# Performance work log

Measured on AMD Instinct MI355X. Metric: run time of the kernel, lower is better.

Reference implementation:

```python
import jax, jax.numpy as jnp
import numpy as np

S = 8192
Q_PARAM = 256
V_PARAM = 256
SCALE = 1.0 / np.sqrt(float(Q_PARAM)).astype(np.float32)


def setup_inputs() -> dict:
    key = jax.random.key(0)
    ks = jax.random.split(key, 12)
    init = lambda k, shape, fan_in: jax.random.uniform(k, shape, jnp.float32, -1.0, 1.0) / np.sqrt(float(fan_in))
    return {
        "query": jax.random.normal(ks[0], (S, Q_PARAM), jnp.float32),
        "key": jax.random.normal(ks[1], (S, Q_PARAM), jnp.float32),
        "value": jax.random.normal(ks[2], (S, V_PARAM), jnp.float32),
        "mask": jax.random.uniform(ks[3], (S, S), jnp.float32),
        "Wq": init(ks[4], (Q_PARAM, Q_PARAM), Q_PARAM),
        "bq": init(ks[5], (Q_PARAM,), Q_PARAM),
        "Wk": init(ks[6], (Q_PARAM, Q_PARAM), Q_PARAM),
        "bk": init(ks[7], (Q_PARAM,), Q_PARAM),
        "Wv": init(ks[8], (V_PARAM, V_PARAM), V_PARAM),
        "bv": init(ks[9], (V_PARAM,), V_PARAM),
        "Wo": init(ks[10], (V_PARAM, V_PARAM), V_PARAM),
        "bo": init(ks[11], (V_PARAM,), V_PARAM),
    }


def reference(query, key, value, mask, Wq, bq, Wk, bk, Wv, bv, Wo, bo):
    # torch nn.Linear: y = x @ W.T + b
    q = query @ Wq.T + bq          # [S, q]
    k = key @ Wk.T + bk            # [S, q]
    v = value @ Wv.T + bv          # [S, v]
    scores = q @ k.T               # [S, S]
    masked = scores * mask         # multiplicative mask BEFORE softmax
    h = jax.nn.softmax(masked * SCALE, axis=1)
    h = h @ v                      # [S, v]
    return h @ Wo.T + bo
```

## Files before the change

### kernel.cpp

```cpp
#include <hip/hip_runtime.h>


#define S 8192
#define NSPLIT 4
#define BM 64
#define BN 32
#define KSPLIT_LEN (S / NSPLIT)
#define NTILES (KSPLIT_LEN / BN)

typedef unsigned short ushort_t;
typedef __attribute__((ext_vector_type(8))) __bf16 bf16x8;
typedef __attribute__((ext_vector_type(4))) float f32x4;
typedef __attribute__((ext_vector_type(4))) ushort_t ushort4_t;
typedef __attribute__((ext_vector_type(8))) ushort_t ushort8_t;

typedef const __attribute__((address_space(1))) unsigned int* gas_u32;
typedef __attribute__((address_space(3))) unsigned int* las_u32;

__device__ __forceinline__ ushort_t f2bf(float f) {
  unsigned u = __builtin_bit_cast(unsigned, f);
  u += 0x7FFFu + ((u >> 16) & 1u);
  return (ushort_t)(u >> 16);
}

__device__ __forceinline__ bf16x8 pack8(f32x4 a, f32x4 b) {
  ushort8_t u;
  u[0] = f2bf(a[0]); u[1] = f2bf(a[1]); u[2] = f2bf(a[2]); u[3] = f2bf(a[3]);
  u[4] = f2bf(b[0]); u[5] = f2bf(b[1]); u[6] = f2bf(b[2]); u[7] = f2bf(b[3]);
  return __builtin_bit_cast(bf16x8, u);
}

__global__ __launch_bounds__(256) void wconv_kernel(
    const float* __restrict__ w0, const float* __restrict__ w1,
    const float* __restrict__ w2, const float* __restrict__ w3,
    ushort_t* __restrict__ o0, ushort_t* __restrict__ o1,
    ushort_t* __restrict__ o2, ushort_t* __restrict__ o3) {
  const int m = blockIdx.y;
  const float* w = (m == 0) ? w0 : (m == 1) ? w1 : (m == 2) ? w2 : w3;
  ushort_t* o = (m == 0) ? o0 : (m == 1) ? o1 : (m == 2) ? o2 : o3;
  const int idx = (blockIdx.x * 256 + threadIdx.x) * 4;
  f32x4 v = *(const f32x4*)(w + idx);
  ushort4_t p;
  p[0] = f2bf(v[0]); p[1] = f2bf(v[1]); p[2] = f2bf(v[2]); p[3] = f2bf(v[3]);
  *(ushort4_t*)(o + idx) = p;
}

template <int IN_BF16, int OUT_MODE>
__global__ __launch_bounds__(256) void proj_kernel(const void* __restrict__ inp,
                                                   const ushort_t* __restrict__ Wb,
                                                   const float* __restrict__ bias,
                                                   void* __restrict__ outp) {
  const int tid = threadIdx.x;
  const int lane = tid & 63;
  const int w = tid >> 6;
  const int lr = lane & 15, lg = lane >> 4;
  const int brow0 = blockIdx.x * 64;
  const int row0 = brow0 + w * 16;
  const int col0 = blockIdx.y * 64;

  f32x4 acc[4] = {};
  const int arow = row0 + lr;
  const int kb = lg * 8;

  bf16x8 af[8];
#pragma unroll
  for (int ks = 0; ks < 8; ++ks) {
    if (IN_BF16) {
      af[ks] = *(const bf16x8*)((const ushort_t*)inp + (size_t)arow * 256 + ks * 32 + kb);
    } else {
      const float* ap = (const float*)inp + (size_t)arow * 256 + ks * 32 + kb;
      af[ks] = pack8(*(const f32x4*)ap, *(const f32x4*)(ap + 4));
    }
  }

#pragma unroll
  for (int ks = 0; ks < 8; ++ks) {
#pragma unroll
    for (int n = 0; n < 4; ++n) {
      bf16x8 bb = *(const bf16x8*)(Wb + (size_t)(col0 + 16 * n + lr) * 256 + ks * 32 + kb);
      acc[n] = __builtin_amdgcn_mfma_f32_16x16x32_bf16(af[ks], bb, acc[n], 0, 0, 0);
    }
  }

  if constexpr (OUT_MODE == 1) {
    __shared__ __align__(16) ushort_t tb[64 * 68];
#pragma unroll
    for (int n = 0; n < 4; ++n) {
      const int col = col0 + 16 * n + lr;
      const float bv = bias[col];
      const int cl = 16 * n + lr;
      const int rowl = w * 16 + lg * 4;
      ushort4_t pk;
#pragma unroll
      for (int r = 0; r < 4; ++r) pk[r] = f2bf(acc[n][r] + bv);
      *(ushort4_t*)&tb[cl * 68 + rowl] = pk;
    }
    __syncthreads();
    ushort_t* o = (ushort_t*)outp;
#pragma unroll
    for (int i = 0; i < 4; ++i) {
      int chunk = i * 256 + tid;
      int c = chunk >> 4;
      int off = (chunk & 15) * 4;
      ushort4_t v0 = *(const ushort4_t*)&tb[c * 68 + off];
      *(ushort4_t*)(o + (size_t)(col0 + c) * S + brow0 + off) = v0;
    }
  } else {
#pragma unroll
    for (int n = 0; n < 4; ++n) {
      const int col = col0 + 16 * n + lr;
      const float bv = bias[col];
      const int rbase = row0 + lg * 4;
      if (OUT_MODE == 0) {
        ushort_t* o = (ushort_t*)outp;
#pragma unroll
        for (int r = 0; r < 4; ++r)
          o[(size_t)(rbase + r) * 256 + col] = f2bf(acc[n][r] + bv);
      } else {
        float* o = (float*)outp;
#pragma unroll
        for (int r = 0; r < 4; ++r)
          o[(size_t)(rbase + r) * 256 + col] = acc[n][r] + bv;
      }
    }
  }
}

__global__ __launch_bounds__(256) void flash_kernel(
    const ushort_t* __restrict__ qb, const ushort_t* __restrict__ kbm,
    const ushort_t* __restrict__ vtb, const float* __restrict__ mask,
    float* __restrict__ Opart, float* __restrict__ lpart) {
  __shared__ __align__(16) ushort_t kt[2 * BN * 256];
  __shared__ __align__(16) ushort_t vt[2 * 256 * BN];
  __shared__ __align__(16) ushort_t pb[4][16 * BN];

  const int tid = threadIdx.x;
  const int lane = tid & 63;
  const int w = tid >> 6;
  const int lr = lane & 15, lg = lane >> 4;
  const int split = blockIdx.y;
  const int kvbase = split * KSPLIT_LEN;
  const int qrow0 = blockIdx.x * BM + w * 16;

  bf16x8 qf[8];
#pragma unroll
  for (int ks = 0; ks < 8; ++ks)
    qf[ks] = *(const bf16x8*)(qb + (size_t)(qrow0 + lr) * 256 + ks * 32 + lg * 8);

  const float* mrow[4];
#pragma unroll
  for (int r = 0; r < 4; ++r)
    mrow[r] = mask + (size_t)(qrow0 + lg * 4 + r) * S + lr;

  f32x4 oacc[16] = {};
  float lsum[4] = {0.f, 0.f, 0.f, 0.f};

  const int pa_off = lr * (BN * 2) + lg * 16;
  const int vt_swz = ((lg ^ (lane & 3)) << 4);
  ushort_t* pbw = &pb[w][0];

  auto stage = [&](int b, int kv0) {
#pragma unroll
    for (int it = 0; it < 4; ++it) {
      int chunk = it * 256 + (w << 6) + lane;
      int r = chunk >> 5;
      int c = (chunk & 31) ^ (r & 7);
      const ushort_t* src = kbm + (size_t)(kv0 + r) * 256 + c * 8;
      __builtin_amdgcn_global_load_lds((gas_u32)src,
                                       (las_u32)(kt + b * 8192 + it * 2048 + w * 512), 16, 0, 0);
    }
#pragma unroll
    for (int it = 0; it < 4; ++it) {
      int chunk = it * 256 + (w << 6) + lane;
      int r = chunk >> 2;
      int c = (chunk & 3) ^ (r & 3);
      const ushort_t* src = vtb + (size_t)r * S + kv0 + c * 8;
      __builtin_amdgcn_global_load_lds((gas_u32)src,
                                       (las_u32)(vt + b * 8192 + it * 2048 + w * 512), 16, 0, 0);
    }
  };

  stage(0, kvbase);
  float mcur[8];
#pragma unroll
  for (int n = 0; n < 2; ++n)
#pragma unroll
    for (int r = 0; r < 4; ++r)
      mcur[n * 4 + r] = __builtin_nontemporal_load(mrow[r] + kvbase + 16 * n);
  __syncthreads();

  for (int t = 0; t < NTILES; ++t) {
    const int cur = t & 1;
    const int tn = (t + 1 < NTILES) ? (t + 1) : t;
    const int kvn = kvbase + tn * BN;

    stage(cur ^ 1, kvn);
    float mnext[8];
#pragma unroll
    for (int n = 0; n < 2; ++n)
#pragma unroll
      for (int r = 0; r < 4; ++r)
        mnext[n * 4 + r] = __builtin_nontemporal_load(mrow[r] + kvn + 16 * n);

    const char* ktc = (const char*)kt + cur * 16384;
    f32x4 sacc[2] = {};
#pragma unroll
    for (int ks = 0; ks < 8; ++ks) {
#pragma unroll
      for (int n = 0; n < 2; ++n) {
        int addr = ((16 * n + lr) << 9) + ((((ks << 2) + lg) ^ (lane & 7)) << 4);
        bf16x8 bk = *(const bf16x8*)(ktc + addr);
        sacc[n] = __builtin_amdgcn_mfma_f32_16x16x32_bf16(qf[ks], bk, sacc[n], 0, 0, 0);
      }
    }

#pragma unroll
    for (int n = 0; n < 2; ++n) {
#pragma unroll
      for (int r = 0; r < 4; ++r) {
        float p = __builtin_amdgcn_exp2f(sacc[n][r] * (mcur[n * 4 + r] * 0.09016844005556021f));
        lsum[r] += p;
        pbw[(lg * 4 + r) * BN + 16 * n + lr] = f2bf(p);
      }
    }

    const char* vtc = (const char*)vt + cur * 16384;
    bf16x8 pa = *(const bf16x8*)((const char*)pbw + pa_off);
#pragma unroll
    for (int nd = 0; nd < 16; ++nd) {
      bf16x8 bv = *(const bf16x8*)(vtc + nd * 1024 + lr * 64 + vt_swz);
      oacc[nd] = __builtin_amdgcn_mfma_f32_16x16x32_bf16(pa, bv, oacc[nd], 0, 0, 0);
    }

#pragma unroll
    for (int i = 0; i < 8; ++i) mcur[i] = mnext[i];
    __syncthreads();
  }

#pragma unroll
  for (int r = 0; r < 4; ++r) {
    float v = lsum[r];
    v += __shfl_xor(v, 1);
    v += __shfl_xor(v, 2);
    v += __shfl_xor(v, 4);
    v += __shfl_xor(v, 8);
    lsum[r] = v;
  }
  const int absrow0 = qrow0 + lg * 4;
  if (lr == 0) {
#pragma unroll
    for (int r = 0; r < 4; ++r)
      lpart[(size_t)split * S + absrow0 + r] = lsum[r];
  }
#pragma unroll
  for (int r = 0; r < 4; ++r) {
    float* orow = Opart + ((size_t)split * S + absrow0 + r) * 256 + lr;
#pragma unroll
    for (int nd = 0; nd < 16; ++nd) orow[nd * 16] = oacc[nd][r];
  }
}

__global__ __launch_bounds__(256) void combine_kernel(const float* __restrict__ Opart,
                                                      const float* __restrict__ lpart,
                                                      ushort_t* __restrict__ hb) {
  const int row = blockIdx.x;
  const int d = threadIdx.x;
  float L = 0.f, acc = 0.f;
#pragma unroll
  for (int s2 = 0; s2 < NSPLIT; ++s2) {
    L += lpart[(size_t)s2 * S + row];
    acc += Opart[((size_t)s2 * S + row) * 256 + d];
  }
  hb[(size_t)row * 256 + d] = f2bf(acc / L);
}

extern "C" void kernel_launch(void* const* d_in, const int* in_sizes, int n_in,
                              void* d_out, int out_size, void* d_ws, size_t ws_size,
                              hipStream_t stream) {
  const float* query = (const float*)d_in[0];
  const float* key   = (const float*)d_in[1];
  const float* value = (const float*)d_in[2];
  const float* mask  = (const float*)d_in[3];
  const float* Wq = (const float*)d_in[4];
  const float* bq = (const float*)d_in[5];
  const float* Wk = (const float*)d_in[6];
  const float* bk = (const float*)d_in[7];
  const float* Wv = (const float*)d_in[8];
  const float* bv = (const float*)d_in[9];
  const float* Wo = (const float*)d_in[10];
  const float* bo = (const float*)d_in[11];

  char* ws = (char*)d_ws;
  ushort_t* qb  = (ushort_t*)(ws);
  ushort_t* kb  = (ushort_t*)(ws + ((size_t)4  << 20));
  ushort_t* vtb = (ushort_t*)(ws + ((size_t)8  << 20));
  ushort_t* hb  = (ushort_t*)(ws + ((size_t)12 << 20));
  float* Opart  = (float*)(ws + ((size_t)16 << 20));
  float* lpart  = (float*)(ws + ((size_t)48 << 20));
  ushort_t* Wqb = (ushort_t*)(ws + ((size_t)49 << 20));
  ushort_t* Wkb = (ushort_t*)(ws + ((size_t)49 << 20) + (128u << 10));
  ushort_t* Wvb = (ushort_t*)(ws + ((size_t)49 << 20) + (256u << 10));
  ushort_t* Wob = (ushort_t*)(ws + ((size_t)49 << 20) + (384u << 10));

  wconv_kernel<<<dim3(64, 4), 256, 0, stream>>>(Wq, Wk, Wv, Wo, Wqb, Wkb, Wvb, Wob);

  dim3 pgrid(S / 64, 4);
  proj_kernel<0, 0><<<pgrid, 256, 0, stream>>>(query, Wqb, bq, qb);
  proj_kernel<0, 0><<<pgrid, 256, 0, stream>>>(key, Wkb, bk, kb);
  proj_kernel<0, 1><<<pgrid, 256, 0, stream>>>(value, Wvb, bv, vtb);

  flash_kernel<<<dim3(S / BM, NSPLIT), 256, 0, stream>>>(qb, kb, vtb, mask, Opart, lpart);

  combine_kernel<<<S, 256, 0, stream>>>(Opart, lpart, hb);

  proj_kernel<1, 2><<<pgrid, 256, 0, stream>>>(hb, Wob, bo, (float*)d_out);
}
```

Before: 225.7 us.

## Restructure flash kernel: 32 rows per wave, register P via permlane, fused QKV

The flash kernel now handles 128 query rows per block, 32 per wave, so each K/V fragment read from LDS feeds two MFMAs. The MFMA operands are swapped so that the P fragment can be built in registers with packed bf16 conversion and permlane swaps, removing the LDS round trip for P. Mask loads are vectorized, the per-tile barrier is replaced by a manual vmcnt wait plus s_barrier, and MFMA sections run at raised priority. The three Q/K/V projections are fused into one launch, and the KV split count is raised to 8 when the workspace is large enough. This adds register pressure under launch_bounds(256,2) and depends on the permlane data layout being correct.

```diff
diff --git a/kernel.cpp b/kernel.cpp
--- a/kernel.cpp
+++ b/kernel.cpp
@@ -2,17 +2,15 @@
 
 
 #define S 8192
-#define NSPLIT 4
-#define BM 64
+#define BM 128
 #define BN 32
-#define KSPLIT_LEN (S / NSPLIT)
-#define NTILES (KSPLIT_LEN / BN)
 
 typedef unsigned short ushort_t;
 typedef __attribute__((ext_vector_type(8))) __bf16 bf16x8;
 typedef __attribute__((ext_vector_type(4))) float f32x4;
 typedef __attribute__((ext_vector_type(4))) ushort_t ushort4_t;
 typedef __attribute__((ext_vector_type(8))) ushort_t ushort8_t;
+typedef __attribute__((ext_vector_type(4))) unsigned uint4_t;
 
 typedef const __attribute__((address_space(1))) unsigned int* gas_u32;
 typedef __attribute__((address_space(3))) unsigned int* las_u32;
@@ -28,6 +26,12 @@
   u[0] = f2bf(a[0]); u[1] = f2bf(a[1]); u[2] = f2bf(a[2]); u[3] = f2bf(a[3]);
   u[4] = f2bf(b[0]); u[5] = f2bf(b[1]); u[6] = f2bf(b[2]); u[7] = f2bf(b[3]);
   return __builtin_bit_cast(bf16x8, u);
+}
+
+__device__ __forceinline__ unsigned cvt_pk_bf16(float lo, float hi) {
+  unsigned r;
+  asm("v_cvt_pk_bf16_f32 %0, %1, %2" : "=v"(r) : "v"(lo), "v"(hi));
+  return r;
 }
 
 __global__ __launch_bounds__(256) void wconv_kernel(
@@ -45,11 +49,21 @@
   *(ushort4_t*)(o + idx) = p;
 }
 
-template <int IN_BF16, int OUT_MODE>
-__global__ __launch_bounds__(256) void proj_kernel(const void* __restrict__ inp,
-                                                   const ushort_t* __restrict__ Wb,
-                                                   const float* __restrict__ bias,
-                                                   void* __restrict__ outp) {
+__global__ __launch_bounds__(256) void qkv_kernel(
+    const float* __restrict__ query, const float* __restrict__ key,
+    const float* __restrict__ value,
+    const ushort_t* __restrict__ Wqb, const ushort_t* __restrict__ Wkb,
+    const ushort_t* __restrict__ Wvb,
+    const float* __restrict__ bq, const float* __restrict__ bk,
+    const float* __restrict__ bv,
+    ushort_t* __restrict__ qo, ushort_t* __restrict__ ko,
+    ushort_t* __restrict__ vto) {
+  __shared__ __align__(16) ushort_t tb[64 * 68];
+  const int z = blockIdx.z;
+  const float* inp = (z == 0) ? query : (z == 1) ? key : value;
+  const ushort_t* Wb = (z == 0) ? Wqb : (z == 1) ? Wkb : Wvb;
+  const float* bias = (z == 0) ? bq : (z == 1) ? bk : bv;
+
   const int tid = threadIdx.x;
   const int lane = tid & 63;
   const int w = tid >> 6;
@@ -65,14 +79,9 @@
   bf16x8 af[8];
 #pragma unroll
   for (int ks = 0; ks < 8; ++ks) {
-    if (IN_BF16) {
-      af[ks] = *(const bf16x8*)((const ushort_t*)inp + (size_t)arow * 256 + ks * 32 + kb);
-    } else {
-      const float* ap = (const float*)inp + (size_t)arow * 256 + ks * 32 + kb;
-      af[ks] = pack8(*(const f32x4*)ap, *(const f32x4*)(ap + 4));
-    }
-  }
-
+    const float* ap = inp + (size_t)arow * 256 + ks * 32 + kb;
+    af[ks] = pack8(*(const f32x4*)ap, *(const f32x4*)(ap + 4));
+  }
 #pragma unroll
   for (int ks = 0; ks < 8; ++ks) {
 #pragma unroll
@@ -82,82 +91,108 @@
     }
   }
 
-  if constexpr (OUT_MODE == 1) {
-    __shared__ __align__(16) ushort_t tb[64 * 68];
+  if (z < 2) {
+    ushort_t* o = z ? ko : qo;
 #pragma unroll
     for (int n = 0; n < 4; ++n) {
       const int col = col0 + 16 * n + lr;
-      const float bv = bias[col];
+      const float bv_ = bias[col];
+      const int rbase = row0 + lg * 4;
+#pragma unroll
+      for (int r = 0; r < 4; ++r)
+        o[(size_t)(rbase + r) * 256 + col] = f2bf(acc[n][r] + bv_);
+    }
+  } else {
+#pragma unroll
+    for (int n = 0; n < 4; ++n) {
+      const int col = col0 + 16 * n + lr;
+      const float bv_ = bias[col];
       const int cl = 16 * n + lr;
       const int rowl = w * 16 + lg * 4;
       ushort4_t pk;
 #pragma unroll
-      for (int r = 0; r < 4; ++r) pk[r] = f2bf(acc[n][r] + bv);
+      for (int r = 0; r < 4; ++r) pk[r] = f2bf(acc[n][r] + bv_);
       *(ushort4_t*)&tb[cl * 68 + rowl] = pk;
     }
     __syncthreads();
-    ushort_t* o = (ushort_t*)outp;
 #pragma unroll
     for (int i = 0; i < 4; ++i) {
       int chunk = i * 256 + tid;
       int c = chunk >> 4;
       int off = (chunk & 15) * 4;
       ushort4_t v0 = *(const ushort4_t*)&tb[c * 68 + off];
-      *(ushort4_t*)(o + (size_t)(col0 + c) * S + brow0 + off) = v0;
-    }
-  } else {
+      *(ushort4_t*)(vto + (size_t)(col0 + c) * S + brow0 + off) = v0;
+    }
+  }
+}
+
+__global__ __launch_bounds__(256) void oproj_kernel(const ushort_t* __restrict__ inp,
+                                                    const ushort_t* __restrict__ Wb,
+                                                    const float* __restrict__ bias,
+                                                    float* __restrict__ outp) {
+  const int tid = threadIdx.x;
+  const int lane = tid & 63;
+  const int w = tid >> 6;
+  const int lr = lane & 15, lg = lane >> 4;
+  const int row0 = blockIdx.x * 64 + w * 16;
+  const int col0 = blockIdx.y * 64;
+
+  f32x4 acc[4] = {};
+  const int arow = row0 + lr;
+  const int kb = lg * 8;
+#pragma unroll
+  for (int ks = 0; ks < 8; ++ks) {
+    bf16x8 a = *(const bf16x8*)(inp + (size_t)arow * 256 + ks * 32 + kb);
 #pragma unroll
     for (int n = 0; n < 4; ++n) {
-      const int col = col0 + 16 * n + lr;
-      const float bv = bias[col];
-      const int rbase = row0 + lg * 4;
-      if (OUT_MODE == 0) {
-        ushort_t* o = (ushort_t*)outp;
-#pragma unroll
-        for (int r = 0; r < 4; ++r)
-          o[(size_t)(rbase + r) * 256 + col] = f2bf(acc[n][r] + bv);
-      } else {
-        float* o = (float*)outp;
-#pragma unroll
-        for (int r = 0; r < 4; ++r)
-          o[(size_t)(rbase + r) * 256 + col] = acc[n][r] + bv;
-      }
-    }
-  }
-}
-
-__global__ __launch_bounds__(256) void flash_kernel(
-    const ushort_t* __restrict__ qb, const ushort_t* __restrict__ kbm,
+      bf16x8 bb = *(const bf16x8*)(Wb + (size_t)(col0 + 16 * n + lr) * 256 + ks * 32 + kb);
+      acc[n] = __builtin_amdgcn_mfma_f32_16x16x32_bf16(a, bb, acc[n], 0, 0, 0);
+    }
+  }
+#pragma unroll
+  for (int n = 0; n < 4; ++n) {
+    const int col = col0 + 16 * n + lr;
+    const float bv = bias[col];
+    const int rbase = row0 + lg * 4;
+#pragma unroll
+    for (int r = 0; r < 4; ++r)
+      outp[(size_t)(rbase + r) * 256 + col] = acc[n][r] + bv;
+  }
+}
+
+template <int NS>
+__global__ __launch_bounds__(256, 2) void flash_kernel(
+    const ushort_t* __restrict__ qg, const ushort_t* __restrict__ kbm,
     const ushort_t* __restrict__ vtb, const float* __restrict__ mask,
     float* __restrict__ Opart, float* __restrict__ lpart) {
-  __shared__ __align__(16) ushort_t kt[2 * BN * 256];
-  __shared__ __align__(16) ushort_t vt[2 * 256 * BN];
-  __shared__ __align__(16) ushort_t pb[4][16 * BN];
+  constexpr int KSPL = S / NS;
+  constexpr int NT = KSPL / BN;
+  __shared__ __align__(16) ushort_t kt[2][BN * 256];
+  __shared__ __align__(16) ushort_t vt[2][256 * BN];
 
   const int tid = threadIdx.x;
   const int lane = tid & 63;
   const int w = tid >> 6;
   const int lr = lane & 15, lg = lane >> 4;
   const int split = blockIdx.y;
-  const int kvbase = split * KSPLIT_LEN;
-  const int qrow0 = blockIdx.x * BM + w * 16;
-
-  bf16x8 qf[8];
-#pragma unroll
-  for (int ks = 0; ks < 8; ++ks)
-    qf[ks] = *(const bf16x8*)(qb + (size_t)(qrow0 + lr) * 256 + ks * 32 + lg * 8);
-
-  const float* mrow[4];
-#pragma unroll
-  for (int r = 0; r < 4; ++r)
-    mrow[r] = mask + (size_t)(qrow0 + lg * 4 + r) * S + lr;
-
-  f32x4 oacc[16] = {};
-  float lsum[4] = {0.f, 0.f, 0.f, 0.f};
-
-  const int pa_off = lr * (BN * 2) + lg * 16;
-  const int vt_swz = ((lg ^ (lane & 3)) << 4);
-  ushort_t* pbw = &pb[w][0];
+  const int kvbase = split * KSPL;
+  const int qrow0 = blockIdx.x * BM + w * 32;
+
+  bf16x8 qf[2][8];
+#pragma unroll
+  for (int qb = 0; qb < 2; ++qb)
+#pragma unroll
+    for (int ks = 0; ks < 8; ++ks)
+      qf[qb][ks] = *(const bf16x8*)(qg + (size_t)(qrow0 + qb * 16 + lr) * 256 + ks * 32 + lg * 8);
+
+  const float* mrow[2];
+#pragma unroll
+  for (int qb = 0; qb < 2; ++qb)
+    mrow[qb] = mask + (size_t)(qrow0 + qb * 16 + lr) * S + lg * 4;
+
+  f32x4 oacc[2][16] = {};
+  float lsum[2] = {0.f, 0.f};
+  const int vt_swz = ((lg ^ (lr & 3)) << 4);
 
   auto stage = [&](int b, int kv0) {
 #pragma unroll
@@ -167,7 +202,7 @@
       int c = (chunk & 31) ^ (r & 7);
       const ushort_t* src = kbm + (size_t)(kv0 + r) * 256 + c * 8;
       __builtin_amdgcn_global_load_lds((gas_u32)src,
-                                       (las_u32)(kt + b * 8192 + it * 2048 + w * 512), 16, 0, 0);
+                                       (las_u32)(&kt[b][0] + it * 2048 + w * 512), 16, 0, 0);
     }
 #pragma unroll
     for (int it = 0; it < 4; ++it) {
@@ -176,90 +211,108 @@
       int c = (chunk & 3) ^ (r & 3);
       const ushort_t* src = vtb + (size_t)r * S + kv0 + c * 8;
       __builtin_amdgcn_global_load_lds((gas_u32)src,
-                                       (las_u32)(vt + b * 8192 + it * 2048 + w * 512), 16, 0, 0);
+                                       (las_u32)(&vt[b][0] + it * 2048 + w * 512), 16, 0, 0);
     }
   };
 
   stage(0, kvbase);
-  float mcur[8];
-#pragma unroll
-  for (int n = 0; n < 2; ++n)
-#pragma unroll
-    for (int r = 0; r < 4; ++r)
-      mcur[n * 4 + r] = __builtin_nontemporal_load(mrow[r] + kvbase + 16 * n);
-  __syncthreads();
-
-  for (int t = 0; t < NTILES; ++t) {
+  f32x4 mcur[2][2];
+#pragma unroll
+  for (int qb = 0; qb < 2; ++qb)
+#pragma unroll
+    for (int kb = 0; kb < 2; ++kb)
+      mcur[qb][kb] = __builtin_nontemporal_load((const f32x4*)(mrow[qb] + kvbase + kb * 16));
+  asm volatile("s_waitcnt vmcnt(4)" ::: "memory");
+  __builtin_amdgcn_s_barrier();
+  __builtin_amdgcn_sched_barrier(0);
+
+  for (int t = 0; t < NT; ++t) {
     const int cur = t & 1;
-    const int tn = (t + 1 < NTILES) ? (t + 1) : t;
-    const int kvn = kvbase + tn * BN;
+    const int kvn = kvbase + ((t + 1 < NT) ? (t + 1) : t) * BN;
 
     stage(cur ^ 1, kvn);
-    float mnext[8];
-#pragma unroll
-    for (int n = 0; n < 2; ++n)
-#pragma unroll
-      for (int r = 0; r < 4; ++r)
-        mnext[n * 4 + r] = __builtin_nontemporal_load(mrow[r] + kvn + 16 * n);
-
-    const char* ktc = (const char*)kt + cur * 16384;
-    f32x4 sacc[2] = {};
+
+    f32x4 sacc[2][2] = {};
+    __builtin_amdgcn_s_setprio(1);
 #pragma unroll
     for (int ks = 0; ks < 8; ++ks) {
 #pragma unroll
-      for (int n = 0; n < 2; ++n) {
-        int addr = ((16 * n + lr) << 9) + ((((ks << 2) + lg) ^ (lane & 7)) << 4);
-        bf16x8 bk = *(const bf16x8*)(ktc + addr);
-        sacc[n] = __builtin_amdgcn_mfma_f32_16x16x32_bf16(qf[ks], bk, sacc[n], 0, 0, 0);
+      for (int kb = 0; kb < 2; ++kb) {
+        int addr = ((kb * 16 + lr) << 9) + ((((ks << 2) + lg) ^ (lr & 7)) << 4);
+        bf16x8 kf = *(const bf16x8*)((const char*)&kt[cur][0] + addr);
+#pragma unroll
+        for (int qb = 0; qb < 2; ++qb)
+          sacc[qb][kb] = __builtin_amdgcn_mfma_f32_16x16x32_bf16(kf, qf[qb][ks], sacc[qb][kb], 0, 0, 0);
       }
     }
-
-#pragma unroll
-    for (int n = 0; n < 2; ++n) {
-#pragma unroll
-      for (int r = 0; r < 4; ++r) {
-        float p = __builtin_amdgcn_exp2f(sacc[n][r] * (mcur[n * 4 + r] * 0.09016844005556021f));
-        lsum[r] += p;
-        pbw[(lg * 4 + r) * BN + 16 * n + lr] = f2bf(p);
-      }
-    }
-
-    const char* vtc = (const char*)vt + cur * 16384;
-    bf16x8 pa = *(const bf16x8*)((const char*)pbw + pa_off);
+    __builtin_amdgcn_s_setprio(0);
+
+    unsigned pw[2][2][2];
+#pragma unroll
+    for (int qb = 0; qb < 2; ++qb) {
+      float p[8];
+#pragma unroll
+      for (int kb = 0; kb < 2; ++kb)
+#pragma unroll
+        for (int r = 0; r < 4; ++r) {
+          float pv = __builtin_amdgcn_exp2f(sacc[qb][kb][r] * (mcur[qb][kb][r] * 0.09016844005556021f));
+          p[kb * 4 + r] = pv;
+          lsum[qb] += pv;
+        }
+      pw[qb][0][0] = cvt_pk_bf16(p[0], p[1]);
+      pw[qb][0][1] = cvt_pk_bf16(p[2], p[3]);
+      pw[qb][1][0] = cvt_pk_bf16(p[4], p[5]);
+      pw[qb][1][1] = cvt_pk_bf16(p[6], p[7]);
+    }
+
+#pragma unroll
+    for (int qb = 0; qb < 2; ++qb)
+#pragma unroll
+      for (int kb = 0; kb < 2; ++kb)
+        mcur[qb][kb] = __builtin_nontemporal_load((const f32x4*)(mrow[qb] + kvn + kb * 16));
+
+    bf16x8 pfrag[2];
+#pragma unroll
+    for (int qb = 0; qb < 2; ++qb) {
+      unsigned a0 = pw[qb][0][0], a1 = pw[qb][0][1];
+      unsigned b0 = pw[qb][1][0], b1 = pw[qb][1][1];
+      asm("v_permlane32_swap_b32 %0, %1" : "+v"(a0), "+v"(b0));
+      asm("v_permlane16_swap_b32 %0, %1" : "+v"(a0), "+v"(b0));
+      asm("v_permlane32_swap_b32 %0, %1" : "+v"(a1), "+v"(b1));
+      asm("v_permlane16_swap_b32 %0, %1" : "+v"(a1), "+v"(b1));
+      uint4_t u = {a0, a1, b0, b1};
+      pfrag[qb] = __builtin_bit_cast(bf16x8, u);
+    }
+
+    __builtin_amdgcn_s_setprio(1);
 #pragma unroll
     for (int nd = 0; nd < 16; ++nd) {
-      bf16x8 bv = *(const bf16x8*)(vtc + nd * 1024 + lr * 64 + vt_swz);
-      oacc[nd] = __builtin_amdgcn_mfma_f32_16x16x32_bf16(pa, bv, oacc[nd], 0, 0, 0);
-    }
-
-#pragma unroll
-    for (int i = 0; i < 8; ++i) mcur[i] = mnext[i];
-    __syncthreads();
-  }
-
-#pragma unroll
-  for (int r = 0; r < 4; ++r) {
-    float v = lsum[r];
-    v += __shfl_xor(v, 1);
-    v += __shfl_xor(v, 2);
-    v += __shfl_xor(v, 4);
-    v += __shfl_xor(v, 8);
-    lsum[r] = v;
-  }
-  const int absrow0 = qrow0 + lg * 4;
-  if (lr == 0) {
-#pragma unroll
-    for (int r = 0; r < 4; ++r)
-      lpart[(size_t)split * S + absrow0 + r] = lsum[r];
-  }
-#pragma unroll
-  for (int r = 0; r < 4; ++r) {
-    float* orow = Opart + ((size_t)split * S + absrow0 + r) * 256 + lr;
-#pragma unroll
-    for (int nd = 0; nd < 16; ++nd) orow[nd * 16] = oacc[nd][r];
-  }
-}
-
+      bf16x8 va = *(const bf16x8*)((const char*)&vt[cur][0] + nd * 1024 + lr * 64 + vt_swz);
+#pragma unroll
+      for (int qb = 0; qb < 2; ++qb)
+        oacc[qb][nd] = __builtin_amdgcn_mfma_f32_16x16x32_bf16(va, pfrag[qb], oacc[qb][nd], 0, 0, 0);
+    }
+    __builtin_amdgcn_s_setprio(0);
+
+    asm volatile("s_waitcnt vmcnt(4)" ::: "memory");
+    __builtin_amdgcn_s_barrier();
+    __builtin_amdgcn_sched_barrier(0);
+  }
+
+#pragma unroll
+  for (int qb = 0; qb < 2; ++qb) {
+    float v = lsum[qb];
+    v += __shfl_xor(v, 16);
+    v += __shfl_xor(v, 32);
+    if (lane < 16)
+      lpart[(size_t)split * S + qrow0 + qb * 16 + lr] = v;
+#pragma unroll
+    for (int nd = 0; nd < 16; ++nd)
+      *(f32x4*)(Opart + ((size_t)split * S + qrow0 + qb * 16 + lr) * 256 + nd * 16 + lg * 4) = oacc[qb][nd];
+  }
+}
+
+template <int NS>
 __global__ __launch_bounds__(256) void combine_kernel(const float* __restrict__ Opart,
                                                       const float* __restrict__ lpart,
                                                       ushort_t* __restrict__ hb) {
@@ -267,7 +320,7 @@
   const int d = threadIdx.x;
   float L = 0.f, acc = 0.f;
 #pragma unroll
-  for (int s2 = 0; s2 < NSPLIT; ++s2) {
+  for (int s2 = 0; s2 < NS; ++s2) {
     L += lpart[(size_t)s2 * S + row];
     acc += Opart[((size_t)s2 * S + row) * 256 + d];
   }
@@ -295,23 +348,28 @@
   ushort_t* kb  = (ushort_t*)(ws + ((size_t)4  << 20));
   ushort_t* vtb = (ushort_t*)(ws + ((size_t)8  << 20));
   ushort_t* hb  = (ushort_t*)(ws + ((size_t)12 << 20));
-  float* Opart  = (float*)(ws + ((size_t)16 << 20));
-  float* lpart  = (float*)(ws + ((size_t)48 << 20));
-  ushort_t* Wqb = (ushort_t*)(ws + ((size_t)49 << 20));
-  ushort_t* Wkb = (ushort_t*)(ws + ((size_t)49 << 20) + (128u << 10));
-  ushort_t* Wvb = (ushort_t*)(ws + ((size_t)49 << 20) + (256u << 10));
-  ushort_t* Wob = (ushort_t*)(ws + ((size_t)49 << 20) + (384u << 10));
+  ushort_t* Wqb = (ushort_t*)(ws + ((size_t)16 << 20));
+  ushort_t* Wkb = (ushort_t*)(ws + ((size_t)16 << 20) + (128u << 10));
+  ushort_t* Wvb = (ushort_t*)(ws + ((size_t)16 << 20) + (256u << 10));
+  ushort_t* Wob = (ushort_t*)(ws + ((size_t)16 << 20) + (384u << 10));
+  float* lpart  = (float*)(ws + ((size_t)16 << 20) + (512u << 10));
+  float* Opart  = (float*)(ws + ((size_t)17 << 20));
+
+  const bool big = ws_size >= ((size_t)82 << 20);
 
   wconv_kernel<<<dim3(64, 4), 256, 0, stream>>>(Wq, Wk, Wv, Wo, Wqb, Wkb, Wvb, Wob);
 
-  dim3 pgrid(S / 64, 4);
-  proj_kernel<0, 0><<<pgrid, 256, 0, stream>>>(query, Wqb, bq, qb);
-  proj_kernel<0, 0><<<pgrid, 256, 0, stream>>>(key, Wkb, bk, kb);
-  proj_kernel<0, 1><<<pgrid, 256, 0, stream>>>(value, Wvb, bv, vtb);
-
-  flash_kernel<<<dim3(S / BM, NSPLIT), 256, 0, stream>>>(qb, kb, vtb, mask, Opart, lpart);
-
-  combine_kernel<<<S, 256, 0, stream>>>(Opart, lpart, hb);
-
-  proj_kernel<1, 2><<<pgrid, 256, 0, stream>>>(hb, Wob, bo, (float*)d_out);
-}
+  qkv_kernel<<<dim3(S / 64, 4, 3), 256, 0, stream>>>(query, key, value,
+                                                     Wqb, Wkb, Wvb, bq, bk, bv,
+                                                     qb, kb, vtb);
+
+  if (big) {
+    flash_kernel<8><<<dim3(S / BM, 8), 256, 0, stream>>>(qb, kb, vtb, mask, Opart, lpart);
+    combine_kernel<8><<<S, 256, 0, stream>>>(Opart, lpart, hb);
+  } else {
+    flash_kernel<4><<<dim3(S / BM, 4), 256, 0, stream>>>(qb, kb, vtb, mask, Opart, lpart);
+    combine_kernel<4><<<S, 256, 0, stream>>>(Opart, lpart, hb);
+  }
+
+  oproj_kernel<<<dim3(S / 64, 4), 256, 0, stream>>>(hb, Wob, bo, (float*)d_out);
+}
```

Result: no change. 225.3 us (-0.1%).
